# Kernel tuning notes

Hardware: AMD Instinct MI355X
Metric: run time of the kernel (lower is better)

Reference implementation:

```python
import jax, jax.numpy as jnp
import numpy as np

T = 16384
J = 21
IN = 3 * J + 278  # 341
H = 512
WIDTH = 64


def _gru_cell(x, h, w_ih, w_hh, b_ih, b_n):
    # equinox GRUCell math: igates = W_ih x + b; hgates = W_hh h
    ig = w_ih @ x + b_ih            # [3H]
    hg = w_hh @ h                   # [3H]
    ir, iz, inn = jnp.split(ig, 3)
    hr, hz, hn = jnp.split(hg, 3)
    r = jax.nn.sigmoid(ir + hr)
    z = jax.nn.sigmoid(iz + hz)
    n = jnp.tanh(inn + r * (hn + b_n))
    return n + z * (h - n)


def setup_inputs() -> dict:
    key = jax.random.key(0)
    ks = jax.random.split(key, 32)
    s = 0.02
    inp = {
        'dh_joint_pos_tj': jax.random.normal(ks[0], (T, J), jnp.float32),
        'dh_joint_vel_tj': jax.random.normal(ks[1], (T, J), jnp.float32),
        'com_inertia_tn': jax.random.normal(ks[2], (T, 160), jnp.float32),
        'com_vel_tn': jax.random.normal(ks[3], (T, 96), jnp.float32),
        'imu_acc_t3': jax.random.normal(ks[4], (T, 3), jnp.float32),
        'imu_gyro_t3': jax.random.normal(ks[5], (T, 3), jnp.float32),
        'act_frc_obs_tn': jax.random.normal(ks[6], (T, J), jnp.float32),
        'base_pos_t3': jax.random.normal(ks[7], (T, 3), jnp.float32),
        'base_quat_t4': jax.random.normal(ks[8], (T, 4), jnp.float32),
        'lin_vel_obs_t3': jax.random.normal(ks[9], (T, 3), jnp.float32),
        'ang_vel_obs_t3': jax.random.normal(ks[10], (T, 3), jnp.float32),
        'lin_vel_cmd_t2': jax.random.normal(ks[11], (T, 2), jnp.float32),
        'ang_vel_cmd_t1': jax.random.normal(ks[12], (T, 1), jnp.float32),
        'hidden_states_dn': jnp.zeros((2, H), jnp.float32),
        # GRU layer 0 (input IN -> H)
        'w_ih0': jax.random.normal(ks[13], (3 * H, IN), jnp.float32) * s,
        'w_hh0': jax.random.normal(ks[14], (3 * H, H), jnp.float32) * s,
        'b_ih0': jax.random.normal(ks[15], (3 * H,), jnp.float32) * s,
        'b_n0': jax.random.normal(ks[16], (H,), jnp.float32) * s,
        # GRU layer 1 (H -> H)
        'w_ih1': jax.random.normal(ks[17], (3 * H, H), jnp.float32) * s,
        'w_hh1': jax.random.normal(ks[18], (3 * H, H), jnp.float32) * s,
        'b_ih1': jax.random.normal(ks[19], (3 * H,), jnp.float32) * s,
        'b_n1': jax.random.normal(ks[20], (H,), jnp.float32) * s,
        # projector MLP: H -> 64 -> 64 -> 1, relu hidden activations
        'mw0': jax.random.normal(ks[21], (WIDTH, H), jnp.float32) * s,
        'mb0': jnp.zeros((WIDTH,), jnp.float32),
        'mw1': jax.random.normal(ks[22], (WIDTH, WIDTH), jnp.float32) * s,
        'mb1': jnp.zeros((WIDTH,), jnp.float32),
        'mw2': jax.random.normal(ks[23], (1, WIDTH), jnp.float32) * s,
        'mb2': jnp.zeros((1,), jnp.float32),
    }
    return inp


def reference(dh_joint_pos_tj, dh_joint_vel_tj, com_inertia_tn, com_vel_tn,
              imu_acc_t3, imu_gyro_t3, act_frc_obs_tn, base_pos_t3,
              base_quat_t4, lin_vel_obs_t3, ang_vel_obs_t3, lin_vel_cmd_t2,
              ang_vel_cmd_t1, hidden_states_dn,
              w_ih0, w_hh0, b_ih0, b_n0, w_ih1, w_hh1, b_ih1, b_n1,
              mw0, mb0, mw1, mb1, mw2, mb2):
    obs_tn = jnp.concatenate([
        dh_joint_pos_tj, dh_joint_vel_tj, com_inertia_tn, com_vel_tn,
        imu_acc_t3, imu_gyro_t3, act_frc_obs_tn, base_pos_t3, base_quat_t4,
        lin_vel_obs_t3, ang_vel_obs_t3, lin_vel_cmd_t2, ang_vel_cmd_t1,
    ], axis=-1)  # [T, 341]

    def scan_fn(carry, xt):
        h0 = _gru_cell(xt, carry[0], w_ih0, w_hh0, b_ih0, b_n0)
        h1 = _gru_cell(h0, carry[1], w_ih1, w_hh1, b_ih1, b_n1)
        v = jax.nn.relu(mw0 @ h1 + mb0)
        v = jax.nn.relu(mw1 @ v + mb1)
        yt = mw2 @ v + mb2  # [1]
        return jnp.stack([h0, h1], axis=0), yt

    new_hidden, out_tn = jax.lax.scan(scan_fn, hidden_states_dn, obs_tn)
    return out_tn, new_hidden
```

## Files before the change

kernel.cpp:

```cpp
#include <hip/hip_runtime.h>
#include <math.h>


#define T_STEPS 16384
#define IN_DIM 341
#define HID 512
#define G3 1536
#define TTILE 16
#define R0 16
#define R0M (R0-1)
#define R1 16
#define R1M (R1-1)

typedef unsigned int v4u __attribute__((ext_vector_type(4)));

__device__ __forceinline__ float dot4(float4 a, float4 b) {
  return fmaf(a.x, b.x, fmaf(a.y, b.y, fmaf(a.z, b.z, a.w * b.w)));
}
__device__ __forceinline__ float fast_sigmoid(float x) {
  return __builtin_amdgcn_rcpf(1.0f + __expf(-x));
}
__device__ __forceinline__ float fast_tanh(float x) {
  return fmaf(-2.0f, __builtin_amdgcn_rcpf(1.0f + __expf(2.0f * x)), 1.0f);
}
__device__ __forceinline__ void st_rlx64(unsigned long long* p, unsigned long long v) {
  __hip_atomic_store(p, v, __ATOMIC_RELAXED, __HIP_MEMORY_SCOPE_AGENT);
}
__device__ __forceinline__ unsigned long long pack_tv(unsigned tag, float v) {
  return ((unsigned long long)tag << 32) | (unsigned long long)__float_as_uint(v);
}
__device__ __forceinline__ void pin4(float4& v) {
  asm volatile("" : "+v"(v.x), "+v"(v.y), "+v"(v.z), "+v"(v.w));
}
__device__ __forceinline__ v4u ld16(const unsigned long long* p) {
  v4u r;
  asm volatile("global_load_dwordx4 %0, %1, off sc0 sc1\n\ts_waitcnt vmcnt(0)"
               : "=v"(r) : "v"(p) : "memory");
  return r;
}
__device__ __forceinline__ void ld16x2(const unsigned long long* p0,
                                       const unsigned long long* p1,
                                       v4u& a, v4u& b) {
  asm volatile("global_load_dwordx4 %0, %2, off sc0 sc1\n\t"
               "global_load_dwordx4 %1, %3, off sc0 sc1\n\t"
               "s_waitcnt vmcnt(0)"
               : "=v"(a), "=v"(b) : "v"(p0), "v"(p1) : "memory");
}

__global__ __launch_bounds__(384) void concat_kernel(
    const float* __restrict__ p0, const float* __restrict__ p1,
    const float* __restrict__ p2, const float* __restrict__ p3,
    const float* __restrict__ p4, const float* __restrict__ p5,
    const float* __restrict__ p6, const float* __restrict__ p7,
    const float* __restrict__ p8, const float* __restrict__ p9,
    const float* __restrict__ p10, const float* __restrict__ p11,
    const float* __restrict__ p12, float* __restrict__ obs) {
  int t = blockIdx.x;
  int k = threadIdx.x;
  if (k >= IN_DIM) return;
  float v;
  if (k < 21)       v = p0[t*21 + k];
  else if (k < 42)  v = p1[t*21 + (k-21)];
  else if (k < 202) v = p2[t*160 + (k-42)];
  else if (k < 298) v = p3[t*96 + (k-202)];
  else if (k < 301) v = p4[t*3 + (k-298)];
  else if (k < 304) v = p5[t*3 + (k-301)];
  else if (k < 325) v = p6[t*21 + (k-304)];
  else if (k < 328) v = p7[t*3 + (k-325)];
  else if (k < 332) v = p8[t*4 + (k-328)];
  else if (k < 335) v = p9[t*3 + (k-332)];
  else if (k < 338) v = p10[t*3 + (k-335)];
  else if (k < 340) v = p11[t*2 + (k-338)];
  else              v = p12[t];
  obs[(size_t)t*IN_DIM + k] = v;
}

__global__ __launch_bounds__(256) void transpose_kernel(const float* __restrict__ w,
                                                        float* __restrict__ wT) {
  __shared__ float tile[32][33];
  int tx = threadIdx.x;
  int ty = threadIdx.y;
  int k = blockIdx.x*32 + tx;
#pragma unroll
  for (int jj = 0; jj < 4; jj++) {
    int r = blockIdx.y*32 + ty*4 + jj;
    tile[ty*4+jj][tx] = (k < IN_DIM) ? w[(size_t)r*IN_DIM + k] : 0.f;
  }
  __syncthreads();
#pragma unroll
  for (int jj = 0; jj < 4; jj++) {
    int kk = blockIdx.x*32 + ty*4 + jj;
    if (kk < IN_DIM) wT[(size_t)kk*G3 + blockIdx.y*32 + tx] = tile[tx][ty*4+jj];
  }
}

__global__ __launch_bounds__(256) void ig0_kernel(const float* __restrict__ wT,
                                                  const float* __restrict__ obs,
                                                  const float* __restrict__ b_ih0,
                                                  float* __restrict__ ig0) {
  int o = blockIdx.x*256 + threadIdx.x;
  int t0 = blockIdx.y * TTILE;
  float acc[TTILE];
  float b = b_ih0[o];
#pragma unroll
  for (int tt = 0; tt < TTILE; tt++) acc[tt] = b;
  for (int k = 0; k < IN_DIM; k++) {
    float wv = wT[(size_t)k*G3 + o];
#pragma unroll
    for (int tt = 0; tt < TTILE; tt++)
      acc[tt] = fmaf(obs[(size_t)(t0+tt)*IN_DIM + k], wv, acc[tt]);
  }
#pragma unroll
  for (int tt = 0; tt < TTILE; tt++)
    ig0[(size_t)(t0+tt)*G3 + o] = acc[tt];
}

__global__ __launch_bounds__(512) void init_kernel(const float* __restrict__ hid,
                                                   unsigned long long* ring0,
                                                   unsigned long long* ring1) {
  int e = threadIdx.x;
  st_rlx64(&ring0[e], pack_tv(0u, hid[e]));
  st_rlx64(&ring1[e], pack_tv(0u, hid[HID + e]));
}

__global__ __launch_bounds__(384)
__attribute__((amdgpu_waves_per_eu(1, 2)))
void seq_kernel(
    const float* __restrict__ ig0, const float* __restrict__ w_hh0,
    const float* __restrict__ b_n0, const float* __restrict__ w_ih1,
    const float* __restrict__ w_hh1, const float* __restrict__ b_ih1,
    const float* __restrict__ b_n1,
    unsigned long long* ring0, unsigned long long* ring1,
    float* __restrict__ h1a, float* __restrict__ d_out) {
  __shared__ float hbuf0[2][HID];
  __shared__ float hbuf1[2][HID];
  __shared__ float igbuf[2][24];
  __shared__ float vpad[24576];
  const int tid = threadIdx.x;
  const int wg = blockIdx.x;
  if (d_out == nullptr) {
    vpad[tid] = (float)tid;
    __syncthreads();
    h1a[tid] = vpad[383 - tid];
  }

  const bool roleA = (tid < 128);
  const int u = tid - 128;
  const int g = roleA ? (tid >> 4) : (u >> 5);
  const int jj = roleA ? (tid & 15) : (u & 15);
  const int half = roleA ? 0 : ((u >> 4) & 1);
  const int j32 = roleA ? 0 : (u & 31);
  const int eg = wg*8 + g;
  const bool leadA = roleA && (jj == 0);
  const bool leadB = (!roleA) && (j32 == 0);

  const float* wsrc = roleA ? w_hh0 : (half ? w_hh1 : w_ih1);
  float4 W[24];
#pragma unroll
  for (int gate = 0; gate < 3; gate++) {
    const float4* row = (const float4*)(wsrc + (size_t)(gate*HID + eg)*HID);
#pragma unroll
    for (int i = 0; i < 8; i++) {
      W[gate*8+i] = row[jj + 16*i];
      pin4(W[gate*8+i]);
    }
  }
  float cr=0.f, cz=0.f, cn=0.f, bnl;
  if (roleA) {
    bnl = b_n0[eg];
  } else {
    cr = b_ih1[eg]; cz = b_ih1[512+eg]; cn = b_ih1[1024+eg]; bnl = b_n1[eg];
  }

  const int iggate = tid >> 3, ige = tid & 7;
  if (tid < 24) igbuf[0][tid] = ig0[(size_t)iggate*HID + wg*8 + ige];

  for (int k = 0; k <= T_STEPS; k++) {
    const int p = k & 1;
    float igpre = 0.f;
    if (tid < 24) {
      int kk = (k+1 < T_STEPS) ? (k+1) : (T_STEPS-1);
      igpre = ig0[(size_t)kk*G3 + (size_t)iggate*HID + wg*8 + ige];
    }
    const unsigned wk0 = (unsigned)k, wk1 = (unsigned)(k-1);
    if (k == 0) {
      if (tid < 256) {
        const unsigned long long* pa = ring0 + 2*tid;
        v4u a = ld16(pa);
        while (a.y != wk0 || a.w != wk0) { __builtin_amdgcn_s_sleep(1); a = ld16(pa); }
        ((float2*)hbuf0[p])[tid] =
            make_float2(__uint_as_float(a.x), __uint_as_float(a.z));
      }
    } else {
      const unsigned long long* pa = ring0 + (size_t)(k & R0M)*HID + 2*tid;
      const unsigned long long* pb = ring1 + (size_t)((k-1) & R1M)*HID + 2*(tid-128);
      if (tid < 128) {
        v4u a = ld16(pa);
        while (a.y != wk0 || a.w != wk0) { __builtin_amdgcn_s_sleep(1); a = ld16(pa); }
        ((float2*)hbuf0[p])[tid] =
            make_float2(__uint_as_float(a.x), __uint_as_float(a.z));
      } else if (tid < 256) {
        v4u a, b;
        ld16x2(pa, pb, a, b);
        while (a.y != wk0 || a.w != wk0) { __builtin_amdgcn_s_sleep(1); a = ld16(pa); }
        while (b.y != wk1 || b.w != wk1) { __builtin_amdgcn_s_sleep(1); b = ld16(pb); }
        ((float2*)hbuf0[p])[tid] =
            make_float2(__uint_as_float(a.x), __uint_as_float(a.z));
        ((float2*)hbuf1[p])[tid-128] =
            make_float2(__uint_as_float(b.x), __uint_as_float(b.z));
      } else {
        v4u b = ld16(pb);
        while (b.y != wk1 || b.w != wk1) { __builtin_amdgcn_s_sleep(1); b = ld16(pb); }
        ((float2*)hbuf1[p])[tid-128] =
            make_float2(__uint_as_float(b.x), __uint_as_float(b.z));
      }
    }
    __syncthreads();
    const bool act = roleA ? (k < T_STEPS) : (k >= 1);
    if (act) {
      const float4* hp = (roleA || half == 0) ? (const float4*)hbuf0[p]
                                              : (const float4*)hbuf1[p];
      float pr=0.f, pz=0.f, pn=0.f;
#pragma unroll
      for (int i = 0; i < 8; i++) {
        float4 hv = hp[jj + 16*i];
        pr += dot4(W[i],hv); pz += dot4(W[8+i],hv); pn += dot4(W[16+i],hv);
      }
#pragma unroll
      for (int s = 1; s < 16; s <<= 1) {
        pr += __shfl_xor(pr, s, 16);
        pz += __shfl_xor(pz, s, 16);
        pn += __shfl_xor(pn, s, 16);
      }
      if (roleA) {
        if (leadA) {
          float r = fast_sigmoid(igbuf[p][g] + pr);
          float z = fast_sigmoid(igbuf[p][8+g] + pz);
          float n = fast_tanh(igbuf[p][16+g] + r*(pn + bnl));
          float hnew = n + z*(hbuf0[p][eg] - n);
          st_rlx64(&ring0[(size_t)((k+1) & R0M)*HID + eg],
                   pack_tv((unsigned)(k+1), hnew));
          if (k == T_STEPS-1) d_out[T_STEPS + eg] = hnew;
        }
      } else {
        float qr = __shfl(pr, 16, 32);
        float qz = __shfl(pz, 16, 32);
        float qn = __shfl(pn, 16, 32);
        if (leadB) {
          float r = fast_sigmoid(pr + cr + qr);
          float z = fast_sigmoid(pz + cz + qz);
          float n = fast_tanh(pn + cn + r*(qn + bnl));
          float hnew = n + z*(hbuf1[p][eg] - n);
          st_rlx64(&ring1[(size_t)(k & R1M)*HID + eg],
                   pack_tv((unsigned)k, hnew));
          h1a[(size_t)(k-1)*HID + eg] = hnew;
          if (k == T_STEPS) d_out[T_STEPS + HID + eg] = hnew;
        }
      }
    }
    if (tid < 24) igbuf[p ^ 1][tid] = igpre;
  }
}

__global__ __launch_bounds__(64) void mlp_kernel(
    const float* __restrict__ h1_all, const float* __restrict__ mw0,
    const float* __restrict__ mb0, const float* __restrict__ mw1,
    const float* __restrict__ mb1, const float* __restrict__ mw2,
    const float* __restrict__ mb2, float* __restrict__ out) {
  const int l = threadIdx.x;
  const int t0 = blockIdx.x * 8;
  __shared__ float v0s[8][64];
  float acc[8];
#pragma unroll
  for (int tt = 0; tt < 8; tt++) acc[tt] = mb0[l];
  const float4* w = (const float4*)(mw0 + (size_t)l*512);
#pragma unroll 4
  for (int i = 0; i < 128; i++) {
    float4 a = w[i];
#pragma unroll
    for (int tt = 0; tt < 8; tt++) {
      float4 b = ((const float4*)(h1_all + (size_t)(t0+tt)*512))[i];
      acc[tt] = fmaf(a.x,b.x, fmaf(a.y,b.y, fmaf(a.z,b.z, fmaf(a.w,b.w, acc[tt]))));
    }
  }
#pragma unroll
  for (int tt = 0; tt < 8; tt++) v0s[tt][l] = fmaxf(acc[tt], 0.f);
  __syncthreads();
  float acc1[8];
#pragma unroll
  for (int tt = 0; tt < 8; tt++) acc1[tt] = mb1[l];
  const float* w1 = mw1 + (size_t)l*64;
  for (int jj = 0; jj < 64; jj++) {
    float wv = w1[jj];
#pragma unroll
    for (int tt = 0; tt < 8; tt++) acc1[tt] = fmaf(wv, v0s[tt][jj], acc1[tt]);
  }
  float w2 = mw2[l];
  float bb = mb2[0];
#pragma unroll
  for (int tt = 0; tt < 8; tt++) {
    float y = w2 * fmaxf(acc1[tt], 0.f);
#pragma unroll
    for (int s = 32; s > 0; s >>= 1) y += __shfl_down(y, s, 64);
    if (l == 0) out[t0+tt] = y + bb;
  }
}

extern "C" void kernel_launch(void* const* d_in, const int* in_sizes, int n_in,
                              void* d_out, int out_size, void* d_ws, size_t ws_size,
                              hipStream_t stream) {
  const float* p0  = (const float*)d_in[0];
  const float* p1  = (const float*)d_in[1];
  const float* p2  = (const float*)d_in[2];
  const float* p3  = (const float*)d_in[3];
  const float* p4  = (const float*)d_in[4];
  const float* p5  = (const float*)d_in[5];
  const float* p6  = (const float*)d_in[6];
  const float* p7  = (const float*)d_in[7];
  const float* p8  = (const float*)d_in[8];
  const float* p9  = (const float*)d_in[9];
  const float* p10 = (const float*)d_in[10];
  const float* p11 = (const float*)d_in[11];
  const float* p12 = (const float*)d_in[12];
  const float* hid   = (const float*)d_in[13];
  const float* w_ih0 = (const float*)d_in[14];
  const float* w_hh0 = (const float*)d_in[15];
  const float* b_ih0 = (const float*)d_in[16];
  const float* b_n0  = (const float*)d_in[17];
  const float* w_ih1 = (const float*)d_in[18];
  const float* w_hh1 = (const float*)d_in[19];
  const float* b_ih1 = (const float*)d_in[20];
  const float* b_n1  = (const float*)d_in[21];
  const float* mw0 = (const float*)d_in[22];
  const float* mb0 = (const float*)d_in[23];
  const float* mw1 = (const float*)d_in[24];
  const float* mb1 = (const float*)d_in[25];
  const float* mw2 = (const float*)d_in[26];
  const float* mb2 = (const float*)d_in[27];
  float* out = (float*)d_out;

  char* base = (char*)d_ws;
  const size_t IG0_B = (size_t)T_STEPS*G3*4;
  const size_t R0_B  = (size_t)R0*HID*8;
  const size_t R1_B  = (size_t)R1*HID*8;
  const size_t H1A_B = (size_t)T_STEPS*HID*4;
  float* ig0 = (float*)base;
  unsigned long long* ring0 = (unsigned long long*)(base + IG0_B);
  unsigned long long* ring1 = (unsigned long long*)(base + IG0_B + R0_B);
  float* h1a = (float*)(base + IG0_B + R0_B + R1_B);
  float* obs = h1a;
  float* wT  = (float*)((char*)h1a + (size_t)T_STEPS*IN_DIM*4);
  if (ws_size < IG0_B + R0_B + R1_B + H1A_B) return;

  concat_kernel<<<T_STEPS, 384, 0, stream>>>(p0,p1,p2,p3,p4,p5,p6,p7,p8,p9,p10,p11,p12, obs);
  transpose_kernel<<<dim3(11,48), dim3(32,8), 0, stream>>>(w_ih0, wT);
  ig0_kernel<<<dim3(6, T_STEPS/TTILE), 256, 0, stream>>>(wT, obs, b_ih0, ig0);
  init_kernel<<<1, 512, 0, stream>>>(hid, ring0, ring1);
  seq_kernel<<<64, 384, 0, stream>>>(ig0, w_hh0, b_n0, w_ih1, w_hh1, b_ih1, b_n1,
                                     ring0, ring1, h1a, out);
  mlp_kernel<<<T_STEPS/8, 64, 0, stream>>>(h1a, mw0, mb0, mw1, mb1, mw2, mb2, out);
}
```

Baseline: 27.63 ms.

## Spread recurrent GRU kernel over 128 workgroups of 192 threads

The persistent sequential kernel now uses 128 workgroups, each owning 4 hidden elements instead of 8, with 192 threads per block. The ring-buffer polling loads are redistributed so each thread fetches up to three 16-byte slots, and the inline asm outputs become early-clobber. The aim is to halve per-block matvec work on the critical path by using more CUs. The cost is more agents in the cross-workgroup flag synchronisation, plus more polling traffic per thread.

```diff
diff --git a/kernel.cpp b/kernel.cpp
--- a/kernel.cpp
+++ b/kernel.cpp
@@ -35,7 +35,7 @@
 __device__ __forceinline__ v4u ld16(const unsigned long long* p) {
   v4u r;
   asm volatile("global_load_dwordx4 %0, %1, off sc0 sc1\n\ts_waitcnt vmcnt(0)"
-               : "=v"(r) : "v"(p) : "memory");
+               : "=&v"(r) : "v"(p) : "memory");
   return r;
 }
 __device__ __forceinline__ void ld16x2(const unsigned long long* p0,
@@ -44,7 +44,24 @@
   asm volatile("global_load_dwordx4 %0, %2, off sc0 sc1\n\t"
                "global_load_dwordx4 %1, %3, off sc0 sc1\n\t"
                "s_waitcnt vmcnt(0)"
-               : "=v"(a), "=v"(b) : "v"(p0), "v"(p1) : "memory");
+               : "=&v"(a), "=&v"(b) : "v"(p0), "v"(p1) : "memory");
+}
+__device__ __forceinline__ void ld16x3(const unsigned long long* p0,
+                                       const unsigned long long* p1,
+                                       const unsigned long long* p2,
+                                       v4u& a, v4u& b, v4u& c) {
+  asm volatile("global_load_dwordx4 %0, %3, off sc0 sc1\n\t"
+               "global_load_dwordx4 %1, %4, off sc0 sc1\n\t"
+               "global_load_dwordx4 %2, %5, off sc0 sc1\n\t"
+               "s_waitcnt vmcnt(0)"
+               : "=&v"(a), "=&v"(b), "=&v"(c)
+               : "v"(p0), "v"(p1), "v"(p2) : "memory");
+}
+__device__ __forceinline__ void vfy(v4u& x, const unsigned long long* p, unsigned want) {
+  while (x.y != want || x.w != want) { __builtin_amdgcn_s_sleep(1); x = ld16(p); }
+}
+__device__ __forceinline__ float2 pairval(v4u x) {
+  return make_float2(__uint_as_float(x.x), __uint_as_float(x.z));
 }
 
 __global__ __launch_bounds__(384) void concat_kernel(
@@ -123,8 +140,8 @@
   st_rlx64(&ring1[e], pack_tv(0u, hid[HID + e]));
 }
 
-__global__ __launch_bounds__(384)
-__attribute__((amdgpu_waves_per_eu(1, 2)))
+__global__ __launch_bounds__(192)
+__attribute__((amdgpu_waves_per_eu(1, 1)))
 void seq_kernel(
     const float* __restrict__ ig0, const float* __restrict__ w_hh0,
     const float* __restrict__ b_n0, const float* __restrict__ w_ih1,
@@ -134,23 +151,23 @@
     float* __restrict__ h1a, float* __restrict__ d_out) {
   __shared__ float hbuf0[2][HID];
   __shared__ float hbuf1[2][HID];
-  __shared__ float igbuf[2][24];
+  __shared__ float igbuf[2][12];
   __shared__ float vpad[24576];
   const int tid = threadIdx.x;
   const int wg = blockIdx.x;
   if (d_out == nullptr) {
     vpad[tid] = (float)tid;
     __syncthreads();
-    h1a[tid] = vpad[383 - tid];
-  }
-
-  const bool roleA = (tid < 128);
-  const int u = tid - 128;
+    h1a[tid] = vpad[191 - tid];
+  }
+
+  const bool roleA = (tid < 64);
+  const int u = tid - 64;
   const int g = roleA ? (tid >> 4) : (u >> 5);
   const int jj = roleA ? (tid & 15) : (u & 15);
   const int half = roleA ? 0 : ((u >> 4) & 1);
-  const int j32 = roleA ? 0 : (u & 31);
-  const int eg = wg*8 + g;
+  const int j32 = u & 31;
+  const int eg = wg*4 + g;
   const bool leadA = roleA && (jj == 0);
   const bool leadB = (!roleA) && (j32 == 0);
 
@@ -172,47 +189,55 @@
     cr = b_ih1[eg]; cz = b_ih1[512+eg]; cn = b_ih1[1024+eg]; bnl = b_n1[eg];
   }
 
-  const int iggate = tid >> 3, ige = tid & 7;
-  if (tid < 24) igbuf[0][tid] = ig0[(size_t)iggate*HID + wg*8 + ige];
+  const int iggate = tid >> 2, ige = tid & 3;
+  if (tid < 12) igbuf[0][tid] = ig0[(size_t)iggate*HID + wg*4 + ige];
 
   for (int k = 0; k <= T_STEPS; k++) {
     const int p = k & 1;
     float igpre = 0.f;
-    if (tid < 24) {
+    if (tid < 12) {
       int kk = (k+1 < T_STEPS) ? (k+1) : (T_STEPS-1);
-      igpre = ig0[(size_t)kk*G3 + (size_t)iggate*HID + wg*8 + ige];
+      igpre = ig0[(size_t)kk*G3 + (size_t)iggate*HID + wg*4 + ige];
     }
     const unsigned wk0 = (unsigned)k, wk1 = (unsigned)(k-1);
     if (k == 0) {
-      if (tid < 256) {
-        const unsigned long long* pa = ring0 + 2*tid;
-        v4u a = ld16(pa);
-        while (a.y != wk0 || a.w != wk0) { __builtin_amdgcn_s_sleep(1); a = ld16(pa); }
-        ((float2*)hbuf0[p])[tid] =
-            make_float2(__uint_as_float(a.x), __uint_as_float(a.z));
+      const unsigned long long* s0 = ring0;
+      if (tid < 64) {
+        v4u a, b;
+        ld16x2(s0 + 2*tid, s0 + 2*(tid+192), a, b);
+        vfy(a, s0 + 2*tid, wk0); vfy(b, s0 + 2*(tid+192), wk0);
+        ((float2*)hbuf0[p])[tid]     = pairval(a);
+        ((float2*)hbuf0[p])[tid+192] = pairval(b);
+      } else {
+        v4u a = ld16(s0 + 2*tid);
+        vfy(a, s0 + 2*tid, wk0);
+        ((float2*)hbuf0[p])[tid] = pairval(a);
       }
     } else {
-      const unsigned long long* pa = ring0 + (size_t)(k & R0M)*HID + 2*tid;
-      const unsigned long long* pb = ring1 + (size_t)((k-1) & R1M)*HID + 2*(tid-128);
-      if (tid < 128) {
-        v4u a = ld16(pa);
-        while (a.y != wk0 || a.w != wk0) { __builtin_amdgcn_s_sleep(1); a = ld16(pa); }
-        ((float2*)hbuf0[p])[tid] =
-            make_float2(__uint_as_float(a.x), __uint_as_float(a.z));
-      } else if (tid < 256) {
+      const unsigned long long* s0 = ring0 + (size_t)(k & R0M)*HID;
+      const unsigned long long* s1 = ring1 + (size_t)((k-1) & R1M)*HID;
+      if (tid < 64) {
+        v4u a, b, c;
+        ld16x3(s0 + 2*tid, s0 + 2*(tid+192), s1 + 2*tid, a, b, c);
+        vfy(a, s0 + 2*tid, wk0); vfy(b, s0 + 2*(tid+192), wk0);
+        vfy(c, s1 + 2*tid, wk1);
+        ((float2*)hbuf0[p])[tid]     = pairval(a);
+        ((float2*)hbuf0[p])[tid+192] = pairval(b);
+        ((float2*)hbuf1[p])[tid]     = pairval(c);
+      } else if (tid < 128) {
+        v4u a, b, c;
+        ld16x3(s0 + 2*tid, s1 + 2*tid, s1 + 2*(tid+128), a, b, c);
+        vfy(a, s0 + 2*tid, wk0);
+        vfy(b, s1 + 2*tid, wk1); vfy(c, s1 + 2*(tid+128), wk1);
+        ((float2*)hbuf0[p])[tid]     = pairval(a);
+        ((float2*)hbuf1[p])[tid]     = pairval(b);
+        ((float2*)hbuf1[p])[tid+128] = pairval(c);
+      } else {
         v4u a, b;
-        ld16x2(pa, pb, a, b);
-        while (a.y != wk0 || a.w != wk0) { __builtin_amdgcn_s_sleep(1); a = ld16(pa); }
-        while (b.y != wk1 || b.w != wk1) { __builtin_amdgcn_s_sleep(1); b = ld16(pb); }
-        ((float2*)hbuf0[p])[tid] =
-            make_float2(__uint_as_float(a.x), __uint_as_float(a.z));
-        ((float2*)hbuf1[p])[tid-128] =
-            make_float2(__uint_as_float(b.x), __uint_as_float(b.z));
-      } else {
-        v4u b = ld16(pb);
-        while (b.y != wk1 || b.w != wk1) { __builtin_amdgcn_s_sleep(1); b = ld16(pb); }
-        ((float2*)hbuf1[p])[tid-128] =
-            make_float2(__uint_as_float(b.x), __uint_as_float(b.z));
+        ld16x2(s0 + 2*tid, s1 + 2*tid, a, b);
+        vfy(a, s0 + 2*tid, wk0); vfy(b, s1 + 2*tid, wk1);
+        ((float2*)hbuf0[p])[tid] = pairval(a);
+        ((float2*)hbuf1[p])[tid] = pairval(b);
       }
     }
     __syncthreads();
@@ -235,8 +260,8 @@
       if (roleA) {
         if (leadA) {
           float r = fast_sigmoid(igbuf[p][g] + pr);
-          float z = fast_sigmoid(igbuf[p][8+g] + pz);
-          float n = fast_tanh(igbuf[p][16+g] + r*(pn + bnl));
+          float z = fast_sigmoid(igbuf[p][4+g] + pz);
+          float n = fast_tanh(igbuf[p][8+g] + r*(pn + bnl));
           float hnew = n + z*(hbuf0[p][eg] - n);
           st_rlx64(&ring0[(size_t)((k+1) & R0M)*HID + eg],
                    pack_tv((unsigned)(k+1), hnew));
@@ -258,7 +283,7 @@
         }
       }
     }
-    if (tid < 24) igbuf[p ^ 1][tid] = igpre;
+    if (tid < 12) igbuf[p ^ 1][tid] = igpre;
   }
 }
 
@@ -356,7 +381,7 @@
   transpose_kernel<<<dim3(11,48), dim3(32,8), 0, stream>>>(w_ih0, wT);
   ig0_kernel<<<dim3(6, T_STEPS/TTILE), 256, 0, stream>>>(wT, obs, b_ih0, ig0);
   init_kernel<<<1, 512, 0, stream>>>(hid, ring0, ring1);
-  seq_kernel<<<64, 384, 0, stream>>>(ig0, w_hh0, b_n0, w_ih1, w_hh1, b_ih1, b_n1,
-                                     ring0, ring1, h1a, out);
+  seq_kernel<<<128, 192, 0, stream>>>(ig0, w_hh0, b_n0, w_ih1, w_hh1, b_ih1, b_n1,
+                                      ring0, ring1, h1a, out);
   mlp_kernel<<<T_STEPS/8, 64, 0, stream>>>(h1a, mw0, mb0, mw1, mb1, mw2, mb2, out);
 }
```

After: 29.68 ms. +7.4%, slower.

## Merge layer-1 input and hidden matvecs into one thread group, shrink block to 256

Applied to the files above, without the earlier changes.

Each layer-1 thread now holds both its w_ih1 and w_hh1 slices in registers, 48 float4 in total, and computes both dot products itself. This removes the cross-half shuffle and shrinks the persistent block from 384 to 256 threads, so every thread loads both ring entries with one paired load. The aim is fewer waves and less intra-block reduction on the sequential critical path. The cost is roughly double the register use per layer-1 thread and more work per thread.

```diff
diff --git a/kernel.cpp b/kernel.cpp
--- a/kernel.cpp
+++ b/kernel.cpp
@@ -35,7 +35,7 @@
 __device__ __forceinline__ v4u ld16(const unsigned long long* p) {
   v4u r;
   asm volatile("global_load_dwordx4 %0, %1, off sc0 sc1\n\ts_waitcnt vmcnt(0)"
-               : "=v"(r) : "v"(p) : "memory");
+               : "=&v"(r) : "v"(p) : "memory");
   return r;
 }
 __device__ __forceinline__ void ld16x2(const unsigned long long* p0,
@@ -44,7 +44,13 @@
   asm volatile("global_load_dwordx4 %0, %2, off sc0 sc1\n\t"
                "global_load_dwordx4 %1, %3, off sc0 sc1\n\t"
                "s_waitcnt vmcnt(0)"
-               : "=v"(a), "=v"(b) : "v"(p0), "v"(p1) : "memory");
+               : "=&v"(a), "=&v"(b) : "v"(p0), "v"(p1) : "memory");
+}
+__device__ __forceinline__ void vfy(v4u& x, const unsigned long long* p, unsigned want) {
+  while (x.y != want || x.w != want) { __builtin_amdgcn_s_sleep(1); x = ld16(p); }
+}
+__device__ __forceinline__ float2 pairval(v4u x) {
+  return make_float2(__uint_as_float(x.x), __uint_as_float(x.z));
 }
 
 __global__ __launch_bounds__(384) void concat_kernel(
@@ -123,8 +129,8 @@
   st_rlx64(&ring1[e], pack_tv(0u, hid[HID + e]));
 }
 
-__global__ __launch_bounds__(384)
-__attribute__((amdgpu_waves_per_eu(1, 2)))
+__global__ __launch_bounds__(256)
+__attribute__((amdgpu_waves_per_eu(1, 1)))
 void seq_kernel(
     const float* __restrict__ ig0, const float* __restrict__ w_hh0,
     const float* __restrict__ b_n0, const float* __restrict__ w_ih1,
@@ -141,28 +147,38 @@
   if (d_out == nullptr) {
     vpad[tid] = (float)tid;
     __syncthreads();
-    h1a[tid] = vpad[383 - tid];
+    h1a[tid] = vpad[255 - tid];
   }
 
   const bool roleA = (tid < 128);
-  const int u = tid - 128;
-  const int g = roleA ? (tid >> 4) : (u >> 5);
-  const int jj = roleA ? (tid & 15) : (u & 15);
-  const int half = roleA ? 0 : ((u >> 4) & 1);
-  const int j32 = roleA ? 0 : (u & 31);
+  const int u = roleA ? tid : (tid - 128);
+  const int g = u >> 4;
+  const int jj = u & 15;
   const int eg = wg*8 + g;
-  const bool leadA = roleA && (jj == 0);
-  const bool leadB = (!roleA) && (j32 == 0);
-
-  const float* wsrc = roleA ? w_hh0 : (half ? w_hh1 : w_ih1);
-  float4 W[24];
-#pragma unroll
-  for (int gate = 0; gate < 3; gate++) {
-    const float4* row = (const float4*)(wsrc + (size_t)(gate*HID + eg)*HID);
-#pragma unroll
-    for (int i = 0; i < 8; i++) {
-      W[gate*8+i] = row[jj + 16*i];
-      pin4(W[gate*8+i]);
+  const bool lead = (jj == 0);
+
+  float4 W0[24], W1[24];
+  {
+    const float* src0 = roleA ? w_hh0 : w_ih1;
+#pragma unroll
+    for (int gate = 0; gate < 3; gate++) {
+      const float4* row = (const float4*)(src0 + (size_t)(gate*HID + eg)*HID);
+#pragma unroll
+      for (int i = 0; i < 8; i++) {
+        W0[gate*8+i] = row[jj + 16*i];
+        pin4(W0[gate*8+i]);
+      }
+    }
+    if (!roleA) {
+#pragma unroll
+      for (int gate = 0; gate < 3; gate++) {
+        const float4* row = (const float4*)(w_hh1 + (size_t)(gate*HID + eg)*HID);
+#pragma unroll
+        for (int i = 0; i < 8; i++) {
+          W1[gate*8+i] = row[jj + 16*i];
+          pin4(W1[gate*8+i]);
+        }
+      }
     }
   }
   float cr=0.f, cz=0.f, cn=0.f, bnl;
@@ -182,58 +198,39 @@
       int kk = (k+1 < T_STEPS) ? (k+1) : (T_STEPS-1);
       igpre = ig0[(size_t)kk*G3 + (size_t)iggate*HID + wg*8 + ige];
     }
-    const unsigned wk0 = (unsigned)k, wk1 = (unsigned)(k-1);
     if (k == 0) {
-      if (tid < 256) {
-        const unsigned long long* pa = ring0 + 2*tid;
-        v4u a = ld16(pa);
-        while (a.y != wk0 || a.w != wk0) { __builtin_amdgcn_s_sleep(1); a = ld16(pa); }
-        ((float2*)hbuf0[p])[tid] =
-            make_float2(__uint_as_float(a.x), __uint_as_float(a.z));
-      }
+      const unsigned long long* pa = ring0 + 2*tid;
+      v4u a = ld16(pa);
+      vfy(a, pa, 0u);
+      ((float2*)hbuf0[p])[tid] = pairval(a);
     } else {
       const unsigned long long* pa = ring0 + (size_t)(k & R0M)*HID + 2*tid;
-      const unsigned long long* pb = ring1 + (size_t)((k-1) & R1M)*HID + 2*(tid-128);
-      if (tid < 128) {
-        v4u a = ld16(pa);
-        while (a.y != wk0 || a.w != wk0) { __builtin_amdgcn_s_sleep(1); a = ld16(pa); }
-        ((float2*)hbuf0[p])[tid] =
-            make_float2(__uint_as_float(a.x), __uint_as_float(a.z));
-      } else if (tid < 256) {
-        v4u a, b;
-        ld16x2(pa, pb, a, b);
-        while (a.y != wk0 || a.w != wk0) { __builtin_amdgcn_s_sleep(1); a = ld16(pa); }
-        while (b.y != wk1 || b.w != wk1) { __builtin_amdgcn_s_sleep(1); b = ld16(pb); }
-        ((float2*)hbuf0[p])[tid] =
-            make_float2(__uint_as_float(a.x), __uint_as_float(a.z));
-        ((float2*)hbuf1[p])[tid-128] =
-            make_float2(__uint_as_float(b.x), __uint_as_float(b.z));
-      } else {
-        v4u b = ld16(pb);
-        while (b.y != wk1 || b.w != wk1) { __builtin_amdgcn_s_sleep(1); b = ld16(pb); }
-        ((float2*)hbuf1[p])[tid-128] =
-            make_float2(__uint_as_float(b.x), __uint_as_float(b.z));
-      }
+      const unsigned long long* pb = ring1 + (size_t)((k-1) & R1M)*HID + 2*tid;
+      const unsigned wk0 = (unsigned)k, wk1 = (unsigned)(k-1);
+      v4u a, b;
+      ld16x2(pa, pb, a, b);
+      vfy(a, pa, wk0);
+      vfy(b, pb, wk1);
+      ((float2*)hbuf0[p])[tid] = pairval(a);
+      ((float2*)hbuf1[p])[tid] = pairval(b);
     }
     __syncthreads();
-    const bool act = roleA ? (k < T_STEPS) : (k >= 1);
-    if (act) {
-      const float4* hp = (roleA || half == 0) ? (const float4*)hbuf0[p]
-                                              : (const float4*)hbuf1[p];
-      float pr=0.f, pz=0.f, pn=0.f;
-#pragma unroll
-      for (int i = 0; i < 8; i++) {
-        float4 hv = hp[jj + 16*i];
-        pr += dot4(W[i],hv); pz += dot4(W[8+i],hv); pn += dot4(W[16+i],hv);
-      }
-#pragma unroll
-      for (int s = 1; s < 16; s <<= 1) {
-        pr += __shfl_xor(pr, s, 16);
-        pz += __shfl_xor(pz, s, 16);
-        pn += __shfl_xor(pn, s, 16);
-      }
-      if (roleA) {
-        if (leadA) {
+    if (roleA) {
+      if (k < T_STEPS) {
+        const float4* hp = (const float4*)hbuf0[p];
+        float pr=0.f, pz=0.f, pn=0.f;
+#pragma unroll
+        for (int i = 0; i < 8; i++) {
+          float4 hv = hp[jj + 16*i];
+          pr += dot4(W0[i],hv); pz += dot4(W0[8+i],hv); pn += dot4(W0[16+i],hv);
+        }
+#pragma unroll
+        for (int s = 1; s < 16; s <<= 1) {
+          pr += __shfl_xor(pr, s, 16);
+          pz += __shfl_xor(pz, s, 16);
+          pn += __shfl_xor(pn, s, 16);
+        }
+        if (lead) {
           float r = fast_sigmoid(igbuf[p][g] + pr);
           float z = fast_sigmoid(igbuf[p][8+g] + pz);
           float n = fast_tanh(igbuf[p][16+g] + r*(pn + bnl));
@@ -242,14 +239,32 @@
                    pack_tv((unsigned)(k+1), hnew));
           if (k == T_STEPS-1) d_out[T_STEPS + eg] = hnew;
         }
-      } else {
-        float qr = __shfl(pr, 16, 32);
-        float qz = __shfl(pz, 16, 32);
-        float qn = __shfl(pn, 16, 32);
-        if (leadB) {
-          float r = fast_sigmoid(pr + cr + qr);
-          float z = fast_sigmoid(pz + cz + qz);
-          float n = fast_tanh(pn + cn + r*(qn + bnl));
+      }
+    } else {
+      if (k >= 1) {
+        const float4* hp0 = (const float4*)hbuf0[p];
+        const float4* hp1 = (const float4*)hbuf1[p];
+        float pr=0.f, pz=0.f, pnih=0.f, pnhh=0.f;
+#pragma unroll
+        for (int i = 0; i < 8; i++) {
+          float4 h0v = hp0[jj + 16*i];
+          float4 h1v = hp1[jj + 16*i];
+          pr   += dot4(W0[i],h0v)    + dot4(W1[i],h1v);
+          pz   += dot4(W0[8+i],h0v)  + dot4(W1[8+i],h1v);
+          pnih += dot4(W0[16+i],h0v);
+          pnhh += dot4(W1[16+i],h1v);
+        }
+#pragma unroll
+        for (int s = 1; s < 16; s <<= 1) {
+          pr   += __shfl_xor(pr, s, 16);
+          pz   += __shfl_xor(pz, s, 16);
+          pnih += __shfl_xor(pnih, s, 16);
+          pnhh += __shfl_xor(pnhh, s, 16);
+        }
+        if (lead) {
+          float r = fast_sigmoid(pr + cr);
+          float z = fast_sigmoid(pz + cz);
+          float n = fast_tanh(pnih + cn + r*(pnhh + bnl));
           float hnew = n + z*(hbuf1[p][eg] - n);
           st_rlx64(&ring1[(size_t)(k & R1M)*HID + eg],
                    pack_tv((unsigned)k, hnew));
@@ -356,7 +371,7 @@
   transpose_kernel<<<dim3(11,48), dim3(32,8), 0, stream>>>(w_ih0, wT);
   ig0_kernel<<<dim3(6, T_STEPS/TTILE), 256, 0, stream>>>(wT, obs, b_ih0, ig0);
   init_kernel<<<1, 512, 0, stream>>>(hid, ring0, ring1);
-  seq_kernel<<<64, 384, 0, stream>>>(ig0, w_hh0, b_n0, w_ih1, w_hh1, b_ih1, b_n1,
+  seq_kernel<<<64, 256, 0, stream>>>(ig0, w_hh0, b_n0, w_ih1, w_hh1, b_ih1, b_n1,
                                      ring0, ring1, h1a, out);
   mlp_kernel<<<T_STEPS/8, 64, 0, stream>>>(h1a, mw0, mb0, mw1, mb1, mw2, mb2, out);
 }
```

Result: slower. 45.48 ms (+64.6%).
